# Kernel optimization log

Hardware: AMD Instinct MI355X
Metric: run time of the kernel (lower is better)

Reference implementation:

```python
import jax, jax.numpy as jnp
import numpy as np

PH, PW = 8, 32          # roi_size (h, w)
NUM_INST = 4
STRIDES = [4, 8, 16, 32]
SR = 2                  # sampling_ratio


def _roi_align(feat, rois, scale):
    """ROIAlign (aligned=False semantics), feat [Nb,C,H,W], rois [N,5] -> [N,C,PH,PW]."""
    Nb, C, H, W = feat.shape
    N = rois.shape[0]
    bid = rois[:, 0].astype(jnp.int32)
    x1 = rois[:, 1] * scale
    y1 = rois[:, 2] * scale
    roi_w = jnp.maximum(rois[:, 3] * scale - x1, 1.0)
    roi_h = jnp.maximum(rois[:, 4] * scale - y1, 1.0)
    # sample coords: y = y1 + (k + 0.5) * bin_h / SR, k in [0, PH*SR)
    ys = y1[:, None] + (jnp.arange(PH * SR, dtype=feat.dtype) + 0.5) * (roi_h / (PH * SR))[:, None]
    xs = x1[:, None] + (jnp.arange(PW * SR, dtype=feat.dtype) + 0.5) * (roi_w / (PW * SR))[:, None]

    def iw(c, size):
        valid = (c >= -1.0) & (c <= size)
        c = jnp.clip(c, 0.0)
        low = jnp.floor(c).astype(jnp.int32)
        atedge = low >= size - 1
        low = jnp.minimum(low, size - 1)
        high = jnp.minimum(low + 1, size - 1)
        frac = jnp.where(atedge, 0.0, c - low.astype(c.dtype))
        return low, high, frac, valid

    yl, yh, fy, vy = iw(ys, H)
    xl, xh, fx, vx = iw(xs, W)

    def gather(yi, xi):
        # advanced indices separated by ':' slice -> result [N, PH*SR, PW*SR, C]
        return feat[bid[:, None, None], :, yi[:, :, None], xi[:, None, :]]

    fy_ = fy[:, :, None, None]
    fx_ = fx[:, None, :, None]
    v = ((1 - fy_) * (1 - fx_) * gather(yl, xl)
         + (1 - fy_) * fx_ * gather(yl, xh)
         + fy_ * (1 - fx_) * gather(yh, xl)
         + fy_ * fx_ * gather(yh, xh))
    v = v * (vy[:, :, None, None] & vx[:, None, :, None]).astype(feat.dtype)
    v = v.reshape(N, PH, SR, PW, SR, C).mean(axis=(2, 4))     # avg over SRxSR samples
    return jnp.transpose(v, (0, 3, 1, 2))                      # [N,C,PH,PW]


def _forward(f0, f1, f2, f3, rois):
    feats = [f0, f1, f2, f3]
    N = rois.shape[0]
    C = f0.shape[1]
    bid = rois[:, 0, 0]
    bx1 = rois[:, :, 1].min(axis=1)
    by1 = rois[:, :, 2].min(axis=1)
    bx2 = rois[:, :, 3].max(axis=1)
    by2 = rois[:, :, 4].max(axis=1)
    bbox = jnp.stack([bid, bx1, by1, bx2, by2], axis=1)        # [N,5]

    # LevelMapper: floor(4 + log2(sqrt(h*w)/224 + eps)), clamp [2,5], minus 2
    s = jnp.sqrt((by2 - by1) * (bx2 - bx1))
    lvl = jnp.floor(4.0 + jnp.log2(s / 224.0 + 1e-6))
    lvl = jnp.clip(lvl, 2.0, 5.0).astype(jnp.int32) - 2        # [N] in 0..3

    rois_feat = jnp.zeros((N, C, PH, PW), dtype=f0.dtype)
    for level, (feat, stride) in enumerate(zip(feats, STRIDES)):
        pooled = _roi_align(feat, bbox, 1.0 / stride)
        rois_feat = jnp.where((lvl == level)[:, None, None, None], pooled, rois_feat)

    # instance masks (vectorized version of the per-ROI slice fills)
    brw = bx2 - bx1
    brh = by2 - by1
    wr = PW / brw
    hr = PH / brh
    ratios = jnp.stack([wr, hr, wr, hr], axis=1)[:, None, :]   # [N,1,4]
    lt = jnp.stack([bx1, by1, bx1, by1], axis=1)[:, None, :]   # [N,1,4]
    pos = ((rois[:, :, 1:] - lt) * ratios).astype(jnp.int32)   # [N,I,4] (x0,y0,x1,y1), trunc == .long()
    rows = jnp.arange(PH)
    cols = jnp.arange(PW)
    mrow = (rows[None, None, :] >= pos[:, :, 1:2]) & (rows[None, None, :] < pos[:, :, 3:4])  # [N,I,PH]
    mcol = (cols[None, None, :] >= pos[:, :, 0:1]) & (cols[None, None, :] < pos[:, :, 2:3])  # [N,I,PW]
    mask = (mrow[:, :, :, None] & mcol[:, :, None, :]).astype(f0.dtype)                      # [N,I,PH,PW]

    out = rois_feat[:, None, :, :, :] * mask[:, :, None, :, :]  # [N,I,C,PH,PW]
    return out.reshape(N, NUM_INST * C, PH, PW)


def setup_inputs() -> dict:
    key = jax.random.key(0)
    ks = jax.random.split(key, 10)
    Nb, C = 2, 256
    f0 = jax.random.normal(ks[0], (Nb, C, 256, 256), dtype=jnp.float32)
    f1 = jax.random.normal(ks[1], (Nb, C, 128, 128), dtype=jnp.float32)
    f2 = jax.random.normal(ks[2], (Nb, C, 64, 64), dtype=jnp.float32)
    f3 = jax.random.normal(ks[3], (Nb, C, 32, 32), dtype=jnp.float32)
    N, I = 256, NUM_INST
    bid = jax.random.randint(ks[4], (N,), 0, Nb).astype(jnp.float32)
    cx = jax.random.uniform(ks[5], (N, I), minval=150.0, maxval=850.0)
    cy = jax.random.uniform(ks[6], (N, I), minval=150.0, maxval=850.0)
    w = jax.random.uniform(ks[7], (N, I), minval=32.0, maxval=280.0)
    h = jax.random.uniform(ks[8], (N, I), minval=16.0, maxval=200.0)
    rois = jnp.stack([jnp.broadcast_to(bid[:, None], (N, I)),
                      cx - w / 2, cy - h / 2, cx + w / 2, cy + h / 2], axis=-1)
    return {"f0": f0, "f1": f1, "f2": f2, "f3": f3, "rois": rois.astype(jnp.float32)}


def reference(f0, f1, f2, f3, rois):
    return _forward(f0, f1, f2, f3, rois)
```

## Files before the change

### kernel.cpp

```cpp
#include <hip/hip_runtime.h>

namespace {

constexpr int NROI  = 256;
constexpr int C     = 256;
constexpr int PHh   = 8;
constexpr int PWw   = 32;
constexpr int NI    = 4;
constexpr int CHUNK = 32;
constexpr int SLAB4_MAX = 512;

__host__ __device__ constexpr unsigned wimm(unsigned vm) {
    return (vm & 0xFu) | (0x7u << 4) | (0xFu << 8) | (((vm >> 4) & 0x3u) << 14);
}

__device__ __forceinline__ void interp_weights(float c, int size,
                                               int& lo, int& hi,
                                               float& w0, float& w1)
{
    bool  valid = (c >= -1.0f) && (c <= (float)size);
    float cc    = fmaxf(c, 0.0f);
    int   low   = (int)floorf(cc);
    bool  atedge = (low >= size - 1);
    low = min(low, size - 1);
    int   high  = min(low + 1, size - 1);
    float frac  = atedge ? 0.0f : (cc - (float)low);
    float v     = valid ? 1.0f : 0.0f;
    lo = low; hi = high;
    w0 = (1.0f - frac) * v;
    w1 = frac * v;
}

template<int K4>
__device__ __forceinline__ void run_staged(
    const float* __restrict__ base, int HW,
    float* b0, float* b1, float* b2,
    const int (&gofs)[2], const int (&toff)[16],
    const float (&tw)[16], const float (&m)[NI],
    float* __restrict__ ob)
{
    auto stage = [&](int ch, float* dst) {
        const float* g = base + (size_t)ch * HW;
        #pragma unroll
        for (int j = 0; j < K4; ++j)
            __builtin_amdgcn_global_load_lds(
                (const __attribute__((address_space(1))) void*)(g + gofs[j]),
                (__attribute__((address_space(3))) void*)(dst + j * 256),
                16, 0, 0);
    };
    auto compute = [&](int cc, const float* lp) {
        float acc = 0.0f;
        #pragma unroll
        for (int k = 0; k < 16; ++k) acc = fmaf(tw[k], lp[toff[k]], acc);
        #pragma unroll
        for (int i = 0; i < NI; ++i)
            __builtin_nontemporal_store(acc * m[i],
                &ob[(size_t)((i * C + cc) * (PHh * PWw))]);
    };

    stage(0, b0); stage(1, b1); stage(2, b2);
    __builtin_amdgcn_s_waitcnt(wimm(2 * K4));
    __builtin_amdgcn_sched_barrier(0);
    compute(0, b0);
    stage(3, b0);
    __builtin_amdgcn_s_waitcnt(wimm(2 * K4 + 4));
    __builtin_amdgcn_sched_barrier(0);
    compute(1, b1);

    float* r0 = b2;
    float* r1 = b0;
    float* r2 = b1;
    #pragma unroll 1
    for (int cc = 2; cc < CHUNK - 2; ++cc) {
        stage(cc + 2, r2);
        __builtin_amdgcn_s_waitcnt(wimm(2 * K4 + 8));
        __builtin_amdgcn_sched_barrier(0);
        compute(cc, r0);
        float* t = r0; r0 = r1; r1 = r2; r2 = t;
    }
    __builtin_amdgcn_s_waitcnt(wimm(K4 + 8));
    __builtin_amdgcn_sched_barrier(0);
    compute(CHUNK - 2, r0);
    __builtin_amdgcn_s_waitcnt(wimm(8));
    __builtin_amdgcn_sched_barrier(0);
    compute(CHUNK - 1, r1);
}

__global__ __launch_bounds__(256) void mia_kernel(
    const float* __restrict__ f0, const float* __restrict__ f1,
    const float* __restrict__ f2, const float* __restrict__ f3,
    const float* __restrict__ rois, float* __restrict__ out)
{
    const int n   = blockIdx.x;
    const int c0  = blockIdx.y * CHUNK;
    const int tid = threadIdx.x;

    __shared__ float sroi[NI * 5];
    __shared__ int   s_ylo[16], s_yhi[16], s_xlo[64], s_xhi[64];
    __shared__ float s_wy0[16], s_wy1[16], s_wx0[64], s_wx1[64];
    __shared__ float wbuf[4][3][SLAB4_MAX];

    if (tid < NI * 5) sroi[tid] = rois[n * (NI * 5) + tid];
    __syncthreads();

    const float bx1 = fminf(fminf(sroi[1],  sroi[6]),  fminf(sroi[11], sroi[16]));
    const float by1 = fminf(fminf(sroi[2],  sroi[7]),  fminf(sroi[12], sroi[17]));
    const float bx2 = fmaxf(fmaxf(sroi[3],  sroi[8]),  fmaxf(sroi[13], sroi[18]));
    const float by2 = fmaxf(fmaxf(sroi[4],  sroi[9]),  fmaxf(sroi[14], sroi[19]));
    const float brw = bx2 - bx1, brh = by2 - by1;

    const float s    = sqrtf(brh * brw);
    const float lv   = floorf(4.0f + log2f(s / 224.0f + 1e-6f));
    const int   level = (int)(fminf(fmaxf(lv, 2.0f), 5.0f)) - 2;

    const float* feat = (level == 0) ? f0 : (level == 1) ? f1 : (level == 2) ? f2 : f3;
    const int   FS    = 256 >> level;
    const float scale = 1.0f / (float)(4 << level);
    const int   bid   = (int)sroi[0];

    const float x1 = bx1 * scale, y1 = by1 * scale;
    const float roi_w = fmaxf(bx2 * scale - x1, 1.0f);
    const float roi_h = fmaxf(by2 * scale - y1, 1.0f);

    if (tid < 16) {
        float bin = roi_h / 16.0f;
        float cy  = y1 + ((float)tid + 0.5f) * bin;
        interp_weights(cy, FS, s_ylo[tid], s_yhi[tid], s_wy0[tid], s_wy1[tid]);
    } else if (tid >= 64 && tid < 128) {
        int   q   = tid - 64;
        float bin = roi_w / 64.0f;
        float cx  = x1 + ((float)q + 0.5f) * bin;
        interp_weights(cx, FS, s_xlo[q], s_xhi[q], s_wx0[q], s_wx1[q]);
    }
    __syncthreads();

    const int ph = tid >> 5, pw = tid & 31;
    const int w  = tid >> 6;

    int   fr[16], fc[16];
    float tw[16];
    {
        int k = 0;
        #pragma unroll
        for (int sr = 0; sr < 2; ++sr) {
            int   r   = 2 * ph + sr;
            int   ylo = s_ylo[r], yhi = s_yhi[r];
            float wy0 = s_wy0[r] * 0.25f, wy1 = s_wy1[r] * 0.25f;
            #pragma unroll
            for (int sc = 0; sc < 2; ++sc) {
                int   q   = 2 * pw + sc;
                int   xlo = s_xlo[q], xhi = s_xhi[q];
                float wx0 = s_wx0[q], wx1 = s_wx1[q];
                fr[k] = ylo; fc[k] = xlo; tw[k] = wy0 * wx0; ++k;
                fr[k] = ylo; fc[k] = xhi; tw[k] = wy0 * wx1; ++k;
                fr[k] = yhi; fc[k] = xlo; tw[k] = wy1 * wx0; ++k;
                fr[k] = yhi; fc[k] = xhi; tw[k] = wy1 * wx1; ++k;
            }
        }
    }

    float m[NI];
    {
        const float wr = (float)PWw / brw;
        const float hr = (float)PHh / brh;
        #pragma unroll
        for (int i = 0; i < NI; ++i) {
            int px0  = (int)((sroi[i * 5 + 1] - bx1) * wr);
            int py1_ = (int)((sroi[i * 5 + 2] - by1) * hr);
            int px2  = (int)((sroi[i * 5 + 3] - bx1) * wr);
            int py3_ = (int)((sroi[i * 5 + 4] - by1) * hr);
            m[i] = (ph >= py1_ && ph < py3_ && pw >= px0 && pw < px2) ? 1.0f : 0.0f;
        }
    }

    const int    HW   = FS * FS;
    const float* base = feat + (size_t)(bid * C + c0) * HW;
    float*       ob   = out + ((size_t)(n * NI) * C + c0) * (PHh * PWw) + tid;

    const int x0     = s_xlo[0];
    const int x0a    = x0 & ~3;
    const int xend   = s_xhi[63] + 1;
    const int Wp4    = (xend - x0a + 3) & ~3;
    const int slabY0 = s_ylo[4 * w];
    const int rowsW  = s_yhi[4 * w + 3] - slabY0 + 1;
    const int slabN4 = rowsW * Wp4;

    if (slabN4 <= SLAB4_MAX) {
        const int K4 = (slabN4 + 255) >> 8;
        const int W4 = Wp4 >> 2;

        int gofs[2];
        {
            const int gmax = (slabN4 >> 2) - 1;
            #pragma unroll
            for (int j = 0; j < 2; ++j) {
                int g = (tid & 63) + j * 64;
                if (g > gmax) g = gmax;
                int row  = g / W4;
                int col4 = g - row * W4;
                gofs[j] = (slabY0 + row) * FS + x0a + (col4 << 2);
            }
        }

        int toff[16];
        #pragma unroll
        for (int k = 0; k < 16; ++k)
            toff[k] = (fr[k] - slabY0) * Wp4 + (fc[k] - x0a);

        float* b0 = &wbuf[w][0][0];
        float* b1 = &wbuf[w][1][0];
        float* b2 = &wbuf[w][2][0];

        if (K4 == 1) run_staged<1>(base, HW, b0, b1, b2, gofs, toff, tw, m, ob);
        else         run_staged<2>(base, HW, b0, b1, b2, gofs, toff, tw, m, ob);
    } else {
        int gidx[16];
        #pragma unroll
        for (int k = 0; k < 16; ++k) gidx[k] = fr[k] * FS + fc[k];

        for (int cc = 0; cc < CHUNK; ++cc) {
            const float* p = base + (size_t)cc * HW;
            float acc = 0.0f;
            #pragma unroll
            for (int k = 0; k < 16; ++k) acc = fmaf(tw[k], p[gidx[k]], acc);
            #pragma unroll
            for (int i = 0; i < NI; ++i)
                __builtin_nontemporal_store(acc * m[i],
                    &ob[(size_t)((i * C + cc) * (PHh * PWw))]);
        }
    }
}

}

extern "C" void kernel_launch(void* const* d_in, const int* in_sizes, int n_in,
                              void* d_out, int out_size, void* d_ws, size_t ws_size,
                              hipStream_t stream)
{
    const float* f0   = (const float*)d_in[0];
    const float* f1   = (const float*)d_in[1];
    const float* f2   = (const float*)d_in[2];
    const float* f3   = (const float*)d_in[3];
    const float* rois = (const float*)d_in[4];
    float*       out  = (float*)d_out;

    dim3 grid(NROI, C / CHUNK);
    mia_kernel<<<grid, 256, 0, stream>>>(f0, f1, f2, f3, rois, out);
}
```

Before: 61.58 us.

## Stage only sampled rows into LDS with interleaved lo/hi row pairs

Each wave's staged LDS slab now holds only the sampled lo/hi row pairs, interleaved per column, instead of a contiguous 16B-aligned rectangle of rows. Loads switch from 16-byte to 4-byte global_load_lds, with up to 10 per stage selected by template. The compute reads float2 pairs (lo row, hi row) from LDS to cut LDS reads in half. The change lets wide or tall ROIs use the staged path rather than the direct-gather fallback, at the cost of many more, narrower global load instructions per channel.

```diff
diff --git a/kernel.cpp b/kernel.cpp
--- a/kernel.cpp
+++ b/kernel.cpp
@@ -8,7 +8,11 @@
 constexpr int PWw   = 32;
 constexpr int NI    = 4;
 constexpr int CHUNK = 32;
-constexpr int SLAB4_MAX = 512;
+constexpr int WP_MAX = 80;
+constexpr int G1P   = 4 * WP_MAX;
+constexpr int KMAXD = (2 * G1P + 63) / 64;
+
+typedef __attribute__((ext_vector_type(2))) float f32x2;
 
 __host__ __device__ constexpr unsigned wimm(unsigned vm) {
     return (vm & 0xFu) | (0x7u << 4) | (0xFu << 8) | (((vm >> 4) & 0x3u) << 14);
@@ -31,27 +35,35 @@
     w1 = frac * v;
 }
 
-template<int K4>
+template<int K>
 __device__ __forceinline__ void run_staged(
     const float* __restrict__ base, int HW,
     float* b0, float* b1, float* b2,
-    const int (&gofs)[2], const int (&toff)[16],
-    const float (&tw)[16], const float (&m)[NI],
+    const int (&gofs)[KMAXD],
+    const int (&toff2)[8], const float (&twt)[16], const float (&m)[NI],
     float* __restrict__ ob)
 {
     auto stage = [&](int ch, float* dst) {
         const float* g = base + (size_t)ch * HW;
         #pragma unroll
-        for (int j = 0; j < K4; ++j)
+        for (int j = 0; j < K; ++j)
             __builtin_amdgcn_global_load_lds(
                 (const __attribute__((address_space(1))) void*)(g + gofs[j]),
-                (__attribute__((address_space(3))) void*)(dst + j * 256),
-                16, 0, 0);
+                (__attribute__((address_space(3))) void*)(dst + j * 64),
+                4, 0, 0);
     };
     auto compute = [&](int cc, const float* lp) {
+        const f32x2* lp2 = (const f32x2*)lp;
         float acc = 0.0f;
         #pragma unroll
-        for (int k = 0; k < 16; ++k) acc = fmaf(tw[k], lp[toff[k]], acc);
+        for (int t = 0; t < 4; ++t) {
+            f32x2 vl = lp2[toff2[2 * t]];
+            f32x2 vh = lp2[toff2[2 * t + 1]];
+            acc = fmaf(twt[4 * t + 0], vl.x, acc);
+            acc = fmaf(twt[4 * t + 1], vl.y, acc);
+            acc = fmaf(twt[4 * t + 2], vh.x, acc);
+            acc = fmaf(twt[4 * t + 3], vh.y, acc);
+        }
         #pragma unroll
         for (int i = 0; i < NI; ++i)
             __builtin_nontemporal_store(acc * m[i],
@@ -59,11 +71,11 @@
     };
 
     stage(0, b0); stage(1, b1); stage(2, b2);
-    __builtin_amdgcn_s_waitcnt(wimm(2 * K4));
+    __builtin_amdgcn_s_waitcnt(wimm(2 * K));
     __builtin_amdgcn_sched_barrier(0);
     compute(0, b0);
     stage(3, b0);
-    __builtin_amdgcn_s_waitcnt(wimm(2 * K4 + 4));
+    __builtin_amdgcn_s_waitcnt(wimm(2 * K + 4));
     __builtin_amdgcn_sched_barrier(0);
     compute(1, b1);
 
@@ -73,12 +85,12 @@
     #pragma unroll 1
     for (int cc = 2; cc < CHUNK - 2; ++cc) {
         stage(cc + 2, r2);
-        __builtin_amdgcn_s_waitcnt(wimm(2 * K4 + 8));
+        __builtin_amdgcn_s_waitcnt(wimm(2 * K + 8));
         __builtin_amdgcn_sched_barrier(0);
         compute(cc, r0);
         float* t = r0; r0 = r1; r1 = r2; r2 = t;
     }
-    __builtin_amdgcn_s_waitcnt(wimm(K4 + 8));
+    __builtin_amdgcn_s_waitcnt(wimm(K + 8));
     __builtin_amdgcn_sched_barrier(0);
     compute(CHUNK - 2, r0);
     __builtin_amdgcn_s_waitcnt(wimm(8));
@@ -98,7 +110,7 @@
     __shared__ float sroi[NI * 5];
     __shared__ int   s_ylo[16], s_yhi[16], s_xlo[64], s_xhi[64];
     __shared__ float s_wy0[16], s_wy1[16], s_wx0[64], s_wx1[64];
-    __shared__ float wbuf[4][3][SLAB4_MAX];
+    __shared__ __align__(16) float wbuf[4][3][2 * G1P];
 
     if (tid < NI * 5) sroi[tid] = rois[n * (NI * 5) + tid];
     __syncthreads();
@@ -137,28 +149,6 @@
     const int ph = tid >> 5, pw = tid & 31;
     const int w  = tid >> 6;
 
-    int   fr[16], fc[16];
-    float tw[16];
-    {
-        int k = 0;
-        #pragma unroll
-        for (int sr = 0; sr < 2; ++sr) {
-            int   r   = 2 * ph + sr;
-            int   ylo = s_ylo[r], yhi = s_yhi[r];
-            float wy0 = s_wy0[r] * 0.25f, wy1 = s_wy1[r] * 0.25f;
-            #pragma unroll
-            for (int sc = 0; sc < 2; ++sc) {
-                int   q   = 2 * pw + sc;
-                int   xlo = s_xlo[q], xhi = s_xhi[q];
-                float wx0 = s_wx0[q], wx1 = s_wx1[q];
-                fr[k] = ylo; fc[k] = xlo; tw[k] = wy0 * wx0; ++k;
-                fr[k] = ylo; fc[k] = xhi; tw[k] = wy0 * wx1; ++k;
-                fr[k] = yhi; fc[k] = xlo; tw[k] = wy1 * wx0; ++k;
-                fr[k] = yhi; fc[k] = xhi; tw[k] = wy1 * wx1; ++k;
-            }
-        }
-    }
-
     float m[NI];
     {
         const float wr = (float)PWw / brw;
@@ -177,47 +167,90 @@
     const float* base = feat + (size_t)(bid * C + c0) * HW;
     float*       ob   = out + ((size_t)(n * NI) * C + c0) * (PHh * PWw) + tid;
 
-    const int x0     = s_xlo[0];
-    const int x0a    = x0 & ~3;
-    const int xend   = s_xhi[63] + 1;
-    const int Wp4    = (xend - x0a + 3) & ~3;
-    const int slabY0 = s_ylo[4 * w];
-    const int rowsW  = s_yhi[4 * w + 3] - slabY0 + 1;
-    const int slabN4 = rowsW * Wp4;
-
-    if (slabN4 <= SLAB4_MAX) {
-        const int K4 = (slabN4 + 255) >> 8;
-        const int W4 = Wp4 >> 2;
-
-        int gofs[2];
-        {
-            const int gmax = (slabN4 >> 2) - 1;
-            #pragma unroll
-            for (int j = 0; j < 2; ++j) {
-                int g = (tid & 63) + j * 64;
-                if (g > gmax) g = gmax;
-                int row  = g / W4;
-                int col4 = g - row * W4;
-                gofs[j] = (slabY0 + row) * FS + x0a + (col4 << 2);
+    const int x0 = s_xlo[0];
+    const int Wp = s_xhi[63] - x0 + 1;
+
+    if (Wp <= WP_MAX) {
+        const int Nd = 8 * Wp;
+        const int K  = (Nd + 63) >> 6;
+
+        int gofs[KMAXD];
+        const float rcpW = 1.0f / (float)Wp;
+        #pragma unroll
+        for (int j = 0; j < KMAXD; ++j) {
+            if (j < K) {
+                int d = (tid & 63) + j * 64;
+                if (d >= Nd) d = Nd - 1;
+                int pr = d >> 1, p = d & 1;
+                int srl = (int)((float)pr * rcpW);
+                int x   = pr - srl * Wp;
+                if (x < 0)        { --srl; x += Wp; }
+                else if (x >= Wp) { ++srl; x -= Wp; }
+                int srg = 4 * w + srl;
+                int row = p ? s_yhi[srg] : s_ylo[srg];
+                gofs[j] = row * FS + x0 + x;
+            } else gofs[j] = 0;
+        }
+
+        int   toff2[8];
+        float twt[16];
+        #pragma unroll
+        for (int dr = 0; dr < 2; ++dr) {
+            int   sr  = 2 * ph + dr;
+            int   srl = sr - 4 * w;
+            float wy0 = s_wy0[sr] * 0.25f, wy1 = s_wy1[sr] * 0.25f;
+            #pragma unroll
+            for (int dq = 0; dq < 2; ++dq) {
+                int q = 2 * pw + dq;
+                int t = dr * 2 + dq;
+                toff2[2 * t]     = srl * Wp + (s_xlo[q] - x0);
+                toff2[2 * t + 1] = srl * Wp + (s_xhi[q] - x0);
+                float wx0 = s_wx0[q], wx1 = s_wx1[q];
+                twt[4 * t + 0] = wy0 * wx0;
+                twt[4 * t + 1] = wy1 * wx0;
+                twt[4 * t + 2] = wy0 * wx1;
+                twt[4 * t + 3] = wy1 * wx1;
             }
         }
-
-        int toff[16];
-        #pragma unroll
-        for (int k = 0; k < 16; ++k)
-            toff[k] = (fr[k] - slabY0) * Wp4 + (fc[k] - x0a);
 
         float* b0 = &wbuf[w][0][0];
         float* b1 = &wbuf[w][1][0];
         float* b2 = &wbuf[w][2][0];
 
-        if (K4 == 1) run_staged<1>(base, HW, b0, b1, b2, gofs, toff, tw, m, ob);
-        else         run_staged<2>(base, HW, b0, b1, b2, gofs, toff, tw, m, ob);
+        switch (K) {
+            case 1:  run_staged<1 >(base, HW, b0, b1, b2, gofs, toff2, twt, m, ob); break;
+            case 2:  run_staged<2 >(base, HW, b0, b1, b2, gofs, toff2, twt, m, ob); break;
+            case 3:  run_staged<3 >(base, HW, b0, b1, b2, gofs, toff2, twt, m, ob); break;
+            case 4:  run_staged<4 >(base, HW, b0, b1, b2, gofs, toff2, twt, m, ob); break;
+            case 5:  run_staged<5 >(base, HW, b0, b1, b2, gofs, toff2, twt, m, ob); break;
+            case 6:  run_staged<6 >(base, HW, b0, b1, b2, gofs, toff2, twt, m, ob); break;
+            case 7:  run_staged<7 >(base, HW, b0, b1, b2, gofs, toff2, twt, m, ob); break;
+            case 8:  run_staged<8 >(base, HW, b0, b1, b2, gofs, toff2, twt, m, ob); break;
+            case 9:  run_staged<9 >(base, HW, b0, b1, b2, gofs, toff2, twt, m, ob); break;
+            default: run_staged<10>(base, HW, b0, b1, b2, gofs, toff2, twt, m, ob); break;
+        }
     } else {
-        int gidx[16];
-        #pragma unroll
-        for (int k = 0; k < 16; ++k) gidx[k] = fr[k] * FS + fc[k];
-
+        int   gidx[16];
+        float tw[16];
+        {
+            int k = 0;
+            #pragma unroll
+            for (int sr = 0; sr < 2; ++sr) {
+                int   r   = 2 * ph + sr;
+                int   ylo = s_ylo[r], yhi = s_yhi[r];
+                float wy0 = s_wy0[r] * 0.25f, wy1 = s_wy1[r] * 0.25f;
+                #pragma unroll
+                for (int sc = 0; sc < 2; ++sc) {
+                    int   q   = 2 * pw + sc;
+                    int   xlo = s_xlo[q], xhi = s_xhi[q];
+                    float wx0 = s_wx0[q], wx1 = s_wx1[q];
+                    gidx[k] = ylo * FS + xlo; tw[k] = wy0 * wx0; ++k;
+                    gidx[k] = ylo * FS + xhi; tw[k] = wy0 * wx1; ++k;
+                    gidx[k] = yhi * FS + xlo; tw[k] = wy1 * wx0; ++k;
+                    gidx[k] = yhi * FS + xhi; tw[k] = wy1 * wx1; ++k;
+                }
+            }
+        }
         for (int cc = 0; cc < CHUNK; ++cc) {
             const float* p = base + (size_t)cc * HW;
             float acc = 0.0f;
```

Measured after the change: 64.02 us. +4.0%, slower.

## Split each ROI block into four single-wavefront blocks over row pairs

Applied to the files above, without the earlier changes.

Each 256-thread block, where four wavefronts each staged their own row-pair slab, becomes a 64-thread block, and a third grid dimension selects the row pair. Each block recomputes the ROI level, x weights and its four y samples, and its LDS use drops to one triple-buffered slab. Wavefronts no longer wait on each other at block barriers, and the smaller blocks should schedule more flexibly and raise occupancy. The cost is four times the blocks, with redundant per-ROI setup and interpolation-weight work in each. The ROI count is now taken from the input size.

```diff
diff --git a/kernel.cpp b/kernel.cpp
--- a/kernel.cpp
+++ b/kernel.cpp
@@ -2,7 +2,6 @@
 
 namespace {
 
-constexpr int NROI  = 256;
 constexpr int C     = 256;
 constexpr int PHh   = 8;
 constexpr int PWw   = 32;
@@ -86,21 +85,22 @@
     compute(CHUNK - 1, r1);
 }
 
-__global__ __launch_bounds__(256) void mia_kernel(
+__global__ __launch_bounds__(64) void mia_kernel(
     const float* __restrict__ f0, const float* __restrict__ f1,
     const float* __restrict__ f2, const float* __restrict__ f3,
     const float* __restrict__ rois, float* __restrict__ out)
 {
-    const int n   = blockIdx.x;
-    const int c0  = blockIdx.y * CHUNK;
-    const int tid = threadIdx.x;
+    const int n    = blockIdx.x;
+    const int c0   = blockIdx.y * CHUNK;
+    const int rp   = blockIdx.z;
+    const int lane = threadIdx.x;
 
     __shared__ float sroi[NI * 5];
-    __shared__ int   s_ylo[16], s_yhi[16], s_xlo[64], s_xhi[64];
-    __shared__ float s_wy0[16], s_wy1[16], s_wx0[64], s_wx1[64];
-    __shared__ float wbuf[4][3][SLAB4_MAX];
-
-    if (tid < NI * 5) sroi[tid] = rois[n * (NI * 5) + tid];
+    __shared__ int   s_ylo[4], s_yhi[4], s_xlo[64], s_xhi[64];
+    __shared__ float s_wy0[4], s_wy1[4], s_wx0[64], s_wx1[64];
+    __shared__ __align__(16) float wbuf[3][SLAB4_MAX];
+
+    if (lane < NI * 5) sroi[lane] = rois[n * (NI * 5) + lane];
     __syncthreads();
 
     const float bx1 = fminf(fminf(sroi[1],  sroi[6]),  fminf(sroi[11], sroi[16]));
@@ -122,20 +122,20 @@
     const float roi_w = fmaxf(bx2 * scale - x1, 1.0f);
     const float roi_h = fmaxf(by2 * scale - y1, 1.0f);
 
-    if (tid < 16) {
+    {
+        float bin = roi_w / 64.0f;
+        float cx  = x1 + ((float)lane + 0.5f) * bin;
+        interp_weights(cx, FS, s_xlo[lane], s_xhi[lane], s_wx0[lane], s_wx1[lane]);
+    }
+    if (lane < 4) {
+        int   r   = 4 * rp + lane;
         float bin = roi_h / 16.0f;
-        float cy  = y1 + ((float)tid + 0.5f) * bin;
-        interp_weights(cy, FS, s_ylo[tid], s_yhi[tid], s_wy0[tid], s_wy1[tid]);
-    } else if (tid >= 64 && tid < 128) {
-        int   q   = tid - 64;
-        float bin = roi_w / 64.0f;
-        float cx  = x1 + ((float)q + 0.5f) * bin;
-        interp_weights(cx, FS, s_xlo[q], s_xhi[q], s_wx0[q], s_wx1[q]);
+        float cy  = y1 + ((float)r + 0.5f) * bin;
+        interp_weights(cy, FS, s_ylo[lane], s_yhi[lane], s_wy0[lane], s_wy1[lane]);
     }
     __syncthreads();
 
-    const int ph = tid >> 5, pw = tid & 31;
-    const int w  = tid >> 6;
+    const int ph = 2 * rp + (lane >> 5), pw = lane & 31;
 
     int   fr[16], fc[16];
     float tw[16];
@@ -143,9 +143,9 @@
         int k = 0;
         #pragma unroll
         for (int sr = 0; sr < 2; ++sr) {
-            int   r   = 2 * ph + sr;
-            int   ylo = s_ylo[r], yhi = s_yhi[r];
-            float wy0 = s_wy0[r] * 0.25f, wy1 = s_wy1[r] * 0.25f;
+            int   lr  = 2 * (lane >> 5) + sr;
+            int   ylo = s_ylo[lr], yhi = s_yhi[lr];
+            float wy0 = s_wy0[lr] * 0.25f, wy1 = s_wy1[lr] * 0.25f;
             #pragma unroll
             for (int sc = 0; sc < 2; ++sc) {
                 int   q   = 2 * pw + sc;
@@ -175,14 +175,15 @@
 
     const int    HW   = FS * FS;
     const float* base = feat + (size_t)(bid * C + c0) * HW;
-    float*       ob   = out + ((size_t)(n * NI) * C + c0) * (PHh * PWw) + tid;
+    float*       ob   = out + ((size_t)(n * NI) * C + c0) * (PHh * PWw)
+                            + ph * PWw + pw;
 
     const int x0     = s_xlo[0];
     const int x0a    = x0 & ~3;
     const int xend   = s_xhi[63] + 1;
     const int Wp4    = (xend - x0a + 3) & ~3;
-    const int slabY0 = s_ylo[4 * w];
-    const int rowsW  = s_yhi[4 * w + 3] - slabY0 + 1;
+    const int slabY0 = s_ylo[0];
+    const int rowsW  = s_yhi[3] - slabY0 + 1;
     const int slabN4 = rowsW * Wp4;
 
     if (slabN4 <= SLAB4_MAX) {
@@ -194,7 +195,7 @@
             const int gmax = (slabN4 >> 2) - 1;
             #pragma unroll
             for (int j = 0; j < 2; ++j) {
-                int g = (tid & 63) + j * 64;
+                int g = lane + j * 64;
                 if (g > gmax) g = gmax;
                 int row  = g / W4;
                 int col4 = g - row * W4;
@@ -207,12 +208,10 @@
         for (int k = 0; k < 16; ++k)
             toff[k] = (fr[k] - slabY0) * Wp4 + (fc[k] - x0a);
 
-        float* b0 = &wbuf[w][0][0];
-        float* b1 = &wbuf[w][1][0];
-        float* b2 = &wbuf[w][2][0];
-
-        if (K4 == 1) run_staged<1>(base, HW, b0, b1, b2, gofs, toff, tw, m, ob);
-        else         run_staged<2>(base, HW, b0, b1, b2, gofs, toff, tw, m, ob);
+        if (K4 == 1) run_staged<1>(base, HW, &wbuf[0][0], &wbuf[1][0], &wbuf[2][0],
+                                   gofs, toff, tw, m, ob);
+        else         run_staged<2>(base, HW, &wbuf[0][0], &wbuf[1][0], &wbuf[2][0],
+                                   gofs, toff, tw, m, ob);
     } else {
         int gidx[16];
         #pragma unroll
@@ -244,6 +243,7 @@
     const float* rois = (const float*)d_in[4];
     float*       out  = (float*)d_out;
 
-    dim3 grid(NROI, C / CHUNK);
-    mia_kernel<<<grid, 256, 0, stream>>>(f0, f1, f2, f3, rois, out);
-}
+    const int nroi = in_sizes[4] / (NI * 5);
+    dim3 grid(nroi, C / CHUNK, PHh / 2);
+    mia_kernel<<<grid, 64, 0, stream>>>(f0, f1, f2, f3, rois, out);
+}
```

Result: slower. 63.27 us (+2.7%).
